# Kernel tuning notes

Hardware: AMD Instinct MI355X
Metric: run time of the kernel (lower is better)

Reference implementation:

```python
import jax, jax.numpy as jnp
import numpy as np

D_MODEL = 768
N_HEADS = 12
D_K = D_MODEL // N_HEADS

def setup_inputs() -> dict:
    key = jax.random.key(0)
    ks = jax.random.split(key, 9)
    B, S = 4, 2048
    s = 1.0 / np.sqrt(D_MODEL)
    return {
        "x": jax.random.normal(ks[0], (B, S, D_MODEL), dtype=jnp.float32),
        "Wq": jax.random.normal(ks[1], (D_MODEL, D_MODEL), dtype=jnp.float32) * s,
        "bq": jnp.zeros((D_MODEL,), dtype=jnp.float32),
        "Wk": jax.random.normal(ks[2], (D_MODEL, D_MODEL), dtype=jnp.float32) * s,
        "bk": jnp.zeros((D_MODEL,), dtype=jnp.float32),
        "Wv": jax.random.normal(ks[3], (D_MODEL, D_MODEL), dtype=jnp.float32) * s,
        "bv": jnp.zeros((D_MODEL,), dtype=jnp.float32),
        "Wo": jax.random.normal(ks[4], (D_MODEL, D_MODEL), dtype=jnp.float32) * s,
        "bo": jnp.zeros((D_MODEL,), dtype=jnp.float32),
    }

def reference(x, Wq, bq, Wk, bk, Wv, bv, Wo, bo):
    B, S, _ = x.shape
    # projections (nn.Linear: x @ W^T + b; here weights stored as (in, out) so x @ W + b)
    q = x @ Wq + bq
    k = x @ Wk + bk
    v = x @ Wv + bv
    # split heads -> (B, H, S, d_k)
    q = q.reshape(B, S, N_HEADS, D_K).transpose(0, 2, 1, 3)
    k = k.reshape(B, S, N_HEADS, D_K).transpose(0, 2, 1, 3)
    v = v.reshape(B, S, N_HEADS, D_K).transpose(0, 2, 1, 3)
    scores = jnp.einsum('bhqd,bhkd->bhqk', q, k) / jnp.sqrt(jnp.float32(D_K))
    causal = jnp.tril(jnp.ones((S, S), dtype=bool))  # True = keep
    scores = jnp.where(causal, scores, jnp.finfo(scores.dtype).min)
    weights = jax.nn.softmax(scores, axis=-1)  # dropout is identity in eval
    out = jnp.einsum('bhqk,bhkd->bhqd', weights, v)
    out = out.transpose(0, 2, 1, 3).reshape(B, S, D_MODEL)
    return out @ Wo + bo
```

## Files before the change

kernel.cpp:

```cpp
#include <hip/hip_runtime.h>
#include <hip/hip_bf16.h>

#define DM    768
#define HEADS 12
#define DK    64
#define SEQ   2048
#define BATCH 4
#define NE    ((size_t)BATCH * SEQ * DM)
#define KT    12
#define BRICK 8192

typedef short v8s __attribute__((ext_vector_type(8)));
typedef float v4f __attribute__((ext_vector_type(4)));

#define LDS_PTR(p) ((__attribute__((address_space(3))) unsigned int*)(p))
#define GLB_PTR(p) ((const __attribute__((address_space(1))) unsigned int*)(p))

__device__ __forceinline__ unsigned short f2bf(float f) {
    union { float f; unsigned u; } v; v.f = f;
    unsigned r = (v.u + 0x7FFFu + ((v.u >> 16) & 1u)) >> 16;
    return (unsigned short)r;
}
__device__ __forceinline__ unsigned pk2(float a, float b) {
    union { float f; unsigned u; } x, y; x.f = a; y.f = b;
    return (x.u >> 16) | (y.u & 0xFFFF0000u);
}
__device__ __forceinline__ unsigned pk2r(float a, float b) {
    return (unsigned)f2bf(a) | ((unsigned)f2bf(b) << 16);
}
__device__ __forceinline__ float fexp2(float x) {
#if __has_builtin(__builtin_amdgcn_exp2f)
    return __builtin_amdgcn_exp2f(x);
#else
    return __expf(x * 0.69314718056f);
#endif
}

#define QSCALE 0.18033688011112042f

__global__ __launch_bounds__(256)
void cvt_x_kernel(const float* __restrict__ x, unsigned short* __restrict__ xb) {
    const size_t p = ((size_t)blockIdx.x * 256 + threadIdx.x) * 8;
    const int m = (int)(p / DM);
    const int k = (int)(p % DM);
    const float4 a = *(const float4*)(x + p);
    const float4 b = *(const float4*)(x + p + 4);
    v8s o;
    o[0] = (short)f2bf(a.x); o[1] = (short)f2bf(a.y);
    o[2] = (short)f2bf(a.z); o[3] = (short)f2bf(a.w);
    o[4] = (short)f2bf(b.x); o[5] = (short)f2bf(b.y);
    o[6] = (short)f2bf(b.z); o[7] = (short)f2bf(b.w);
    const size_t dst = ((size_t)(m >> 7) * KT + (k >> 6)) * BRICK + (size_t)(m & 127) * 64 + (k & 63);
    *(v8s*)(xb + dst) = o;
}

__global__ __launch_bounds__(256)
void cvt_w_kernel(const float* __restrict__ W0, const float* __restrict__ W1,
                  const float* __restrict__ W2, const float* __restrict__ W3,
                  unsigned short* __restrict__ wt) {
    __shared__ unsigned short T[64][72];
    const int z = blockIdx.z;
    const float* W = (z == 0) ? W0 : (z == 1) ? W1 : (z == 2) ? W2 : W3;
    const float scale = (z == 0) ? QSCALE : 1.0f;
    const int k0 = blockIdx.x * 64, n0 = blockIdx.y * 64;
    const int t = threadIdx.x;
    {
        const int kr = t >> 2;
        const int ns = (t & 3) * 16;
        #pragma unroll
        for (int j = 0; j < 4; ++j) {
            const float4 v = *(const float4*)(W + (size_t)(k0 + kr) * DM + n0 + ns + j * 4);
            T[ns + j * 4 + 0][kr] = f2bf(v.x * scale);
            T[ns + j * 4 + 1][kr] = f2bf(v.y * scale);
            T[ns + j * 4 + 2][kr] = f2bf(v.z * scale);
            T[ns + j * 4 + 3][kr] = f2bf(v.w * scale);
        }
    }
    __syncthreads();
    {
        unsigned short* dst = wt + (size_t)z * DM * DM +
            ((size_t)(n0 >> 7) * KT + (k0 >> 6)) * BRICK + (size_t)(n0 & 64) * 64;
        const int n = t >> 2;
        const int ks = (t & 3) * 16;
        #pragma unroll
        for (int j = 0; j < 2; ++j)
            *(v8s*)(dst + (size_t)n * 64 + ks + j * 8) = *(const v8s*)&T[n][ks + j * 8];
    }
}

__global__ __launch_bounds__(256)
void gemm_qkv_kernel(const unsigned short* __restrict__ xb, const unsigned short* __restrict__ wtbuf,
                     const float* __restrict__ bq, const float* __restrict__ bk,
                     const float* __restrict__ bv,
                     unsigned short* __restrict__ qb, unsigned short* __restrict__ kb,
                     unsigned short* __restrict__ vtb) {
    __shared__ unsigned short smem[32768];
    const int idx = blockIdx.x;
    const int xcd = idx & 7, g = idx >> 3;
    const int mb = xcd + 8 * (g & 7);
    const int yb = g >> 3;
    const int z = yb / 6;
    const int N0 = (yb % 6) * 128;
    const float* bias = (z == 0) ? bq : (z == 1) ? bk : bv;
    const float bscale = (z == 0) ? QSCALE : 1.0f;

    const int t = threadIdx.x;
    const int w = t >> 6, lane = t & 63, quad = lane >> 4, l15 = lane & 15;
    const int wm = w >> 1, wn = w & 1;
    const int M0 = mb * 128;

    const unsigned short* gA = xb + (size_t)mb * (KT * BRICK);
    const unsigned short* gB = wtbuf + (size_t)yb * (KT * BRICK);

    const int r8 = lane >> 3;
    const int c8 = (lane & 7) ^ r8;
    const int goff = r8 * 64 + c8 * 8;
    const int rl = l15 & 7, rh = l15 >> 3;

    v4f acc[4][4];
    #pragma unroll
    for (int i = 0; i < 4; ++i)
        #pragma unroll
        for (int j = 0; j < 4; ++j) acc[i][j] = (v4f){0, 0, 0, 0};

    #pragma unroll
    for (int u = 0; u < 4; ++u) {
        const int win = w * 4 + u;
        __builtin_amdgcn_global_load_lds(GLB_PTR(gA + win * 512 + goff), LDS_PTR(smem + win * 512), 16, 0, 0);
        __builtin_amdgcn_global_load_lds(GLB_PTR(gB + win * 512 + goff), LDS_PTR(smem + 16384 + win * 512), 16, 0, 0);
    }
    __syncthreads();

    for (int kt = 0; kt < KT; ++kt) {
        const int cur = kt & 1;
        if (kt + 1 < KT) {
            const unsigned short* ta = gA + (kt + 1) * BRICK;
            const unsigned short* tb = gB + (kt + 1) * BRICK;
            const int nb = (1 - cur) * 8192;
            #pragma unroll
            for (int u = 0; u < 4; ++u) {
                const int win = w * 4 + u;
                __builtin_amdgcn_global_load_lds(GLB_PTR(ta + win * 512 + goff), LDS_PTR(smem + nb + win * 512), 16, 0, 0);
                __builtin_amdgcn_global_load_lds(GLB_PTR(tb + win * 512 + goff), LDS_PTR(smem + 16384 + nb + win * 512), 16, 0, 0);
            }
        }
        const unsigned short* As = smem + cur * 8192;
        const unsigned short* Bs = smem + 16384 + cur * 8192;
        #pragma unroll
        for (int kc = 0; kc < 2; ++kc) {
            const int cs = ((kc << 2) | quad) ^ rl;
            v8s a[4], b[4];
            #pragma unroll
            for (int i = 0; i < 4; ++i)
                a[i] = *(const v8s*)&As[(wm * 8 + i * 2 + rh) * 512 + rl * 64 + cs * 8];
            #pragma unroll
            for (int j = 0; j < 4; ++j)
                b[j] = *(const v8s*)&Bs[(wn * 8 + j * 2 + rh) * 512 + rl * 64 + cs * 8];
            #pragma unroll
            for (int i = 0; i < 4; ++i)
                #pragma unroll
                for (int j = 0; j < 4; ++j)
                    acc[i][j] = __builtin_amdgcn_mfma_f32_16x16x32_bf16(a[i], b[j], acc[i][j], 0, 0, 0);
        }
        __syncthreads();
    }

    const int b_ = M0 >> 11;
    const int sidx0 = M0 & 2047;
    const int h0 = N0 >> 6;

    if (z < 2) {
        unsigned short* outp = (z == 0) ? qb : kb;
        #pragma unroll
        for (int j = 0; j < 4; ++j) {
            const int n = N0 + wn * 64 + j * 16 + l15;
            const int h = n >> 6, d = n & 63;
            const float bv_ = bias[n] * bscale;
            #pragma unroll
            for (int i = 0; i < 4; ++i)
                #pragma unroll
                for (int r = 0; r < 4; ++r) {
                    const int sidx = sidx0 + wm * 64 + i * 16 + quad * 4 + r;
                    outp[(((size_t)(b_ * HEADS + h) * SEQ + sidx) << 6) + d] = f2bf(acc[i][j][r] + bv_);
                }
        }
    } else {
        unsigned short* Ts = smem;
        #pragma unroll
        for (int p = 0; p < 2; ++p) {
            __syncthreads();
            if (wm == p) {
                #pragma unroll
                for (int j = 0; j < 4; ++j) {
                    const int dloc = wn * 64 + j * 16 + l15;
                    const float bv_ = bias[N0 + dloc];
                    #pragma unroll
                    for (int i = 0; i < 4; ++i)
                        #pragma unroll
                        for (int r = 0; r < 4; ++r)
                            Ts[dloc * 72 + i * 16 + quad * 4 + r] = f2bf(acc[i][j][r] + bv_);
                }
            }
            __syncthreads();
            const int dloc = t >> 1, ms = (t & 1) * 32;
            const int h = h0 + (dloc >> 6), d = dloc & 63;
            unsigned short* dst = vtb + (((size_t)(b_ * HEADS + h) * DK + d) << 11) + sidx0 + p * 64 + ms;
            #pragma unroll
            for (int jj = 0; jj < 4; ++jj)
                *(v8s*)(dst + jj * 8) = *(const v8s*)&Ts[dloc * 72 + ms + jj * 8];
        }
    }
}

__global__ __launch_bounds__(256)
void gemm_out_kernel(const unsigned short* __restrict__ ob, const unsigned short* __restrict__ wto,
                     const float* __restrict__ bias, float* __restrict__ out) {
    __shared__ unsigned short smem[32768];
    const int idx = blockIdx.x;
    const int xcd = idx & 7, g = idx >> 3;
    const int mb = xcd + 8 * (g & 7);
    const int nb = g >> 3;
    const int t = threadIdx.x;
    const int w = t >> 6, lane = t & 63, quad = lane >> 4, l15 = lane & 15;
    const int wm = w >> 1, wn = w & 1;
    const int M0 = mb * 128;
    const int N0 = nb * 128;

    const unsigned short* gA = ob + (size_t)mb * (KT * BRICK);
    const unsigned short* gB = wto + (size_t)nb * (KT * BRICK);

    const int r8 = lane >> 3;
    const int c8 = (lane & 7) ^ r8;
    const int goff = r8 * 64 + c8 * 8;
    const int rl = l15 & 7, rh = l15 >> 3;

    v4f acc[4][4];
    #pragma unroll
    for (int i = 0; i < 4; ++i)
        #pragma unroll
        for (int j = 0; j < 4; ++j) acc[i][j] = (v4f){0, 0, 0, 0};

    #pragma unroll
    for (int u = 0; u < 4; ++u) {
        const int win = w * 4 + u;
        __builtin_amdgcn_global_load_lds(GLB_PTR(gA + win * 512 + goff), LDS_PTR(smem + win * 512), 16, 0, 0);
        __builtin_amdgcn_global_load_lds(GLB_PTR(gB + win * 512 + goff), LDS_PTR(smem + 16384 + win * 512), 16, 0, 0);
    }
    __syncthreads();

    for (int kt = 0; kt < KT; ++kt) {
        const int cur = kt & 1;
        if (kt + 1 < KT) {
            const unsigned short* ta = gA + (kt + 1) * BRICK;
            const unsigned short* tb = gB + (kt + 1) * BRICK;
            const int nxt = (1 - cur) * 8192;
            #pragma unroll
            for (int u = 0; u < 4; ++u) {
                const int win = w * 4 + u;
                __builtin_amdgcn_global_load_lds(GLB_PTR(ta + win * 512 + goff), LDS_PTR(smem + nxt + win * 512), 16, 0, 0);
                __builtin_amdgcn_global_load_lds(GLB_PTR(tb + win * 512 + goff), LDS_PTR(smem + 16384 + nxt + win * 512), 16, 0, 0);
            }
        }
        const unsigned short* As = smem + cur * 8192;
        const unsigned short* Bs = smem + 16384 + cur * 8192;
        #pragma unroll
        for (int kc = 0; kc < 2; ++kc) {
            const int cs = ((kc << 2) | quad) ^ rl;
            v8s a[4], b[4];
            #pragma unroll
            for (int i = 0; i < 4; ++i)
                a[i] = *(const v8s*)&As[(wm * 8 + i * 2 + rh) * 512 + rl * 64 + cs * 8];
            #pragma unroll
            for (int j = 0; j < 4; ++j)
                b[j] = *(const v8s*)&Bs[(wn * 8 + j * 2 + rh) * 512 + rl * 64 + cs * 8];
            #pragma unroll
            for (int i = 0; i < 4; ++i)
                #pragma unroll
                for (int j = 0; j < 4; ++j)
                    acc[i][j] = __builtin_amdgcn_mfma_f32_16x16x32_bf16(a[i], b[j], acc[i][j], 0, 0, 0);
        }
        __syncthreads();
    }

    #pragma unroll
    for (int j = 0; j < 4; ++j) {
        const int n = N0 + wn * 64 + j * 16 + l15;
        const float bv_ = bias[n];
        #pragma unroll
        for (int i = 0; i < 4; ++i)
            #pragma unroll
            for (int r = 0; r < 4; ++r) {
                const int m = M0 + wm * 64 + i * 16 + quad * 4 + r;
                out[(size_t)m * DM + n] = acc[i][j][r] + bv_;
            }
    }
}

__global__ __launch_bounds__(256, 5)
void attn_kernel(const unsigned short* __restrict__ Q, const unsigned short* __restrict__ K,
                 const unsigned short* __restrict__ VT, unsigned short* __restrict__ O) {
    __shared__ unsigned short smem[16384];
    unsigned short* Kb = smem;
    unsigned short* Vb = smem + 4096;
    unsigned short* Ps = smem + 8192;
    const int t = threadIdx.x;
    const int w = t >> 6, lane = t & 63, quad = lane >> 4, l15 = lane & 15;
    const int e7 = l15 & 7;

    const int idx = blockIdx.x;
    const int xcd = idx & 7;
    const int g   = idx >> 3;
    const int bh  = xcd + 8 * (g % 6);
    const int s   = 31 - g / 6;
    const int q0  = s * 64;
    const int nkt = s + 1;
    const size_t kvbase = (size_t)bh * SEQ * DK;

    v8s qf[2];
    #pragma unroll
    for (int c = 0; c < 2; ++c)
        qf[c] = *(const v8s*)(Q + kvbase + (size_t)(q0 + w * 16 + l15) * DK + c * 32 + quad * 8);

    v4f o[4];
    #pragma unroll
    for (int nf = 0; nf < 4; ++nf) o[nf] = (v4f){0, 0, 0, 0};
    v4f os = (v4f){0, 0, 0, 0};
    const v4f zero4 = (v4f){0, 0, 0, 0};

    const short one_bf = (short)0x3F80;
    const v8s ones = (v8s){one_bf, one_bf, one_bf, one_bf, one_bf, one_bf, one_bf, one_bf};

    const int srow = t >> 3;
    const int sc16 = t & 7;
    const int scolsw = (sc16 ^ (srow & 7)) * 8;
    const int gcol = sc16 * 8;
    const int so0 = srow * 64 + scolsw;
    const int so1 = (srow + 32) * 64 + scolsw;

    v8s kr0 = *(const v8s*)(K  + kvbase + (size_t)srow * DK + gcol);
    v8s kr1 = *(const v8s*)(K  + kvbase + (size_t)(srow + 32) * DK + gcol);
    v8s vr0 = *(const v8s*)(VT + kvbase + ((size_t)srow << 11) + gcol);
    v8s vr1 = *(const v8s*)(VT + kvbase + ((size_t)(srow + 32) << 11) + gcol);
    *(v8s*)&Kb[so0] = kr0;
    *(v8s*)&Kb[so1] = kr1;
    *(v8s*)&Vb[so0] = vr0;
    *(v8s*)&Vb[so1] = vr1;
    __syncthreads();

    const int q_ = q0 + w * 16 + l15;
    unsigned short* Pw = Ps + w * 1024;

    for (int kt = 0; kt < nkt; ++kt) {
        const int k0 = kt * 64;
        if (kt + 1 < nkt) {
            const int kn = k0 + 64;
            kr0 = *(const v8s*)(K  + kvbase + (size_t)(kn + srow) * DK + gcol);
            kr1 = *(const v8s*)(K  + kvbase + (size_t)(kn + srow + 32) * DK + gcol);
            vr0 = *(const v8s*)(VT + kvbase + ((size_t)srow << 11) + kn + gcol);
            vr1 = *(const v8s*)(VT + kvbase + ((size_t)(srow + 32) << 11) + kn + gcol);
        }

        v4f sc[4];
        #pragma unroll
        for (int s4 = 0; s4 < 4; ++s4) {
            const v8s kf = *(const v8s*)&Kb[(s4 * 16 + l15) * 64 + (quad ^ e7) * 8];
            sc[s4] = __builtin_amdgcn_mfma_f32_16x16x32_bf16(kf, qf[0], zero4, 0, 0, 0);
        }
        #pragma unroll
        for (int s4 = 0; s4 < 4; ++s4) {
            const v8s kf = *(const v8s*)&Kb[(s4 * 16 + l15) * 64 + ((4 | quad) ^ e7) * 8];
            sc[s4] = __builtin_amdgcn_mfma_f32_16x16x32_bf16(kf, qf[1], sc[s4], 0, 0, 0);
        }

        {
            const bool msk = (kt == s);
            #pragma unroll
            for (int s4 = 0; s4 < 4; ++s4) {
                float p[4];
                #pragma unroll
                for (int r = 0; r < 4; ++r) p[r] = fexp2(sc[s4][r]);
                if (msk) {
                    #pragma unroll
                    for (int r = 0; r < 4; ++r) {
                        const int key = k0 + s4 * 16 + quad * 4 + r;
                        if (key > q_) p[r] = 0.f;
                    }
                }
                uint2 pkv; pkv.x = pk2(p[0], p[1]); pkv.y = pk2(p[2], p[3]);
                const int col8 = (s4 * 4 + quad) ^ (e7 << 1);
                *(uint2*)&Pw[l15 * 64 + col8 * 4] = pkv;
            }
        }

        #pragma unroll
        for (int kc = 0; kc < 2; ++kc) {
            const int c16 = ((kc * 4 + quad) ^ e7) * 8;
            const v8s pf = *(const v8s*)&Pw[l15 * 64 + c16];
            os = __builtin_amdgcn_mfma_f32_16x16x32_bf16(ones, pf, os, 0, 0, 0);
            #pragma unroll
            for (int nf = 0; nf < 4; ++nf) {
                const v8s vf = *(const v8s*)&Vb[(nf * 16 + l15) * 64 + c16];
                o[nf] = __builtin_amdgcn_mfma_f32_16x16x32_bf16(vf, pf, o[nf], 0, 0, 0);
            }
        }

        if (kt + 1 < nkt) {
            __syncthreads();
            *(v8s*)&Kb[so0] = kr0;
            *(v8s*)&Kb[so1] = kr1;
            *(v8s*)&Vb[so0] = vr0;
            *(v8s*)&Vb[so1] = vr1;
            __syncthreads();
        }
    }

    const float inv = 1.f / os[0];

    const int b = bh / HEADS, h = bh % HEADS;
    const size_t br = ((size_t)(b * 16 + (q0 >> 7)) * KT + h) * BRICK;
    const int rowl = (q0 & 127) + w * 16 + l15;
    #pragma unroll
    for (int nf = 0; nf < 4; ++nf) {
        uint2 a2;
        a2.x = pk2r(o[nf][0] * inv, o[nf][1] * inv);
        a2.y = pk2r(o[nf][2] * inv, o[nf][3] * inv);
        *(uint2*)(O + br + (size_t)rowl * 64 + nf * 16 + quad * 4) = a2;
    }
}

extern "C" void kernel_launch(void* const* d_in, const int* in_sizes, int n_in,
                              void* d_out, int out_size, void* d_ws, size_t ws_size,
                              hipStream_t stream) {
    const float* x  = (const float*)d_in[0];
    const float* Wq = (const float*)d_in[1];
    const float* bq = (const float*)d_in[2];
    const float* Wk = (const float*)d_in[3];
    const float* bk = (const float*)d_in[4];
    const float* Wv = (const float*)d_in[5];
    const float* bv = (const float*)d_in[6];
    const float* Wo = (const float*)d_in[7];
    const float* bo = (const float*)d_in[8];
    float* out = (float*)d_out;

    unsigned short* xb  = (unsigned short*)d_ws;
    unsigned short* qb  = xb  + NE;
    unsigned short* kb  = qb  + NE;
    unsigned short* vtb = kb  + NE;
    unsigned short* wt  = vtb + NE;
    unsigned short* ob  = xb;

    cvt_x_kernel<<<dim3(NE / (8 * 256)), 256, 0, stream>>>(x, xb);
    cvt_w_kernel<<<dim3(12, 12, 4), 256, 0, stream>>>(Wq, Wk, Wv, Wo, wt);
    gemm_qkv_kernel<<<dim3(1152), 256, 0, stream>>>(xb, wt, bq, bk, bv, qb, kb, vtb);
    attn_kernel<<<dim3(1536), 256, 0, stream>>>(qb, kb, vtb, ob);
    gemm_out_kernel<<<dim3(384), 256, 0, stream>>>(ob, wt + (size_t)3 * DM * DM, bo, out);
}
```

Baseline: 200.4 us.

## Keep P in registers via 16x16x16 MFMA and double-buffer K/V tiles

```diff
diff --git a/kernel.cpp b/kernel.cpp
--- a/kernel.cpp
+++ b/kernel.cpp
@@ -10,6 +10,7 @@
 #define KT    12
 #define BRICK 8192
 
+typedef short v4s __attribute__((ext_vector_type(4)));
 typedef short v8s __attribute__((ext_vector_type(8)));
 typedef float v4f __attribute__((ext_vector_type(4)));
 
@@ -33,6 +34,17 @@
     return __builtin_amdgcn_exp2f(x);
 #else
     return __expf(x * 0.69314718056f);
+#endif
+}
+__device__ __forceinline__ v4f mfma16(v4s a, v4s b, v4f c) {
+#if __has_builtin(__builtin_amdgcn_mfma_f32_16x16x16_bf16)
+    return __builtin_amdgcn_mfma_f32_16x16x16_bf16(a, b, c, 0, 0, 0);
+#elif __has_builtin(__builtin_amdgcn_mfma_f32_16x16x16bf16_1k)
+    return __builtin_amdgcn_mfma_f32_16x16x16bf16_1k(a, b, c, 0, 0, 0);
+#else
+    v4f d;
+    asm("v_mfma_f32_16x16x16_bf16 %0, %1, %2, %3" : "=&v"(d) : "v"(a), "v"(b), "v"(c));
+    return d;
 #endif
 }
 
@@ -300,12 +312,10 @@
 void attn_kernel(const unsigned short* __restrict__ Q, const unsigned short* __restrict__ K,
                  const unsigned short* __restrict__ VT, unsigned short* __restrict__ O) {
     __shared__ unsigned short smem[16384];
-    unsigned short* Kb = smem;
-    unsigned short* Vb = smem + 4096;
-    unsigned short* Ps = smem + 8192;
     const int t = threadIdx.x;
     const int w = t >> 6, lane = t & 63, quad = lane >> 4, l15 = lane & 15;
     const int e7 = l15 & 7;
+    const int q1 = quad >> 1, q0x = quad & 1;
 
     const int idx = blockIdx.x;
     const int xcd = idx & 7;
@@ -328,7 +338,7 @@
     const v4f zero4 = (v4f){0, 0, 0, 0};
 
     const short one_bf = (short)0x3F80;
-    const v8s ones = (v8s){one_bf, one_bf, one_bf, one_bf, one_bf, one_bf, one_bf, one_bf};
+    const v4s ones4 = (v4s){one_bf, one_bf, one_bf, one_bf};
 
     const int srow = t >> 3;
     const int sc16 = t & 7;
@@ -341,15 +351,15 @@
     v8s kr1 = *(const v8s*)(K  + kvbase + (size_t)(srow + 32) * DK + gcol);
     v8s vr0 = *(const v8s*)(VT + kvbase + ((size_t)srow << 11) + gcol);
     v8s vr1 = *(const v8s*)(VT + kvbase + ((size_t)(srow + 32) << 11) + gcol);
-    *(v8s*)&Kb[so0] = kr0;
-    *(v8s*)&Kb[so1] = kr1;
-    *(v8s*)&Vb[so0] = vr0;
-    *(v8s*)&Vb[so1] = vr1;
+    *(v8s*)&smem[so0]        = kr0;
+    *(v8s*)&smem[so1]        = kr1;
+    *(v8s*)&smem[8192 + so0] = vr0;
+    *(v8s*)&smem[8192 + so1] = vr1;
     __syncthreads();
 
     const int q_ = q0 + w * 16 + l15;
-    unsigned short* Pw = Ps + w * 1024;
-
+
+    int cur = 0;
     for (int kt = 0; kt < nkt; ++kt) {
         const int k0 = kt * 64;
         if (kt + 1 < nkt) {
@@ -359,19 +369,22 @@
             vr0 = *(const v8s*)(VT + kvbase + ((size_t)srow << 11) + kn + gcol);
             vr1 = *(const v8s*)(VT + kvbase + ((size_t)(srow + 32) << 11) + kn + gcol);
         }
+        const unsigned short* Kc = smem + cur * 4096;
+        const unsigned short* Vc = smem + 8192 + cur * 4096;
 
         v4f sc[4];
         #pragma unroll
         for (int s4 = 0; s4 < 4; ++s4) {
-            const v8s kf = *(const v8s*)&Kb[(s4 * 16 + l15) * 64 + (quad ^ e7) * 8];
+            const v8s kf = *(const v8s*)&Kc[(s4 * 16 + l15) * 64 + ((quad ^ e7) << 3)];
             sc[s4] = __builtin_amdgcn_mfma_f32_16x16x32_bf16(kf, qf[0], zero4, 0, 0, 0);
         }
         #pragma unroll
         for (int s4 = 0; s4 < 4; ++s4) {
-            const v8s kf = *(const v8s*)&Kb[(s4 * 16 + l15) * 64 + ((4 | quad) ^ e7) * 8];
+            const v8s kf = *(const v8s*)&Kc[(s4 * 16 + l15) * 64 + (((4 | quad) ^ e7) << 3)];
             sc[s4] = __builtin_amdgcn_mfma_f32_16x16x32_bf16(kf, qf[1], sc[s4], 0, 0, 0);
         }
 
+        v4s pa[4];
         {
             const bool msk = (kt == s);
             #pragma unroll
@@ -386,46 +399,48 @@
                         if (key > q_) p[r] = 0.f;
                     }
                 }
-                uint2 pkv; pkv.x = pk2(p[0], p[1]); pkv.y = pk2(p[2], p[3]);
-                const int col8 = (s4 * 4 + quad) ^ (e7 << 1);
-                *(uint2*)&Pw[l15 * 64 + col8 * 4] = pkv;
-            }
-        }
-
-        #pragma unroll
-        for (int kc = 0; kc < 2; ++kc) {
-            const int c16 = ((kc * 4 + quad) ^ e7) * 8;
-            const v8s pf = *(const v8s*)&Pw[l15 * 64 + c16];
-            os = __builtin_amdgcn_mfma_f32_16x16x32_bf16(ones, pf, os, 0, 0, 0);
-            #pragma unroll
-            for (int nf = 0; nf < 4; ++nf) {
-                const v8s vf = *(const v8s*)&Vb[(nf * 16 + l15) * 64 + c16];
-                o[nf] = __builtin_amdgcn_mfma_f32_16x16x32_bf16(vf, pf, o[nf], 0, 0, 0);
-            }
-        }
+                union { unsigned u[2]; v4s s; } pu;
+                pu.u[0] = pk2(p[0], p[1]); pu.u[1] = pk2(p[2], p[3]);
+                pa[s4] = pu.s;
+            }
+        }
+
+        #pragma unroll
+        for (int nf = 0; nf < 4; ++nf) {
+            const int rowb = (nf * 16 + l15) * 64;
+            #pragma unroll
+            for (int s4 = 0; s4 < 4; ++s4) {
+                const v4s vb = *(const v4s*)&Vc[rowb + (((2 * s4 + q1) ^ e7) << 3) + (q0x << 2)];
+                o[nf] = mfma16(pa[s4], vb, o[nf]);
+            }
+        }
+        #pragma unroll
+        for (int s4 = 0; s4 < 4; ++s4)
+            os = mfma16(pa[s4], ones4, os);
 
         if (kt + 1 < nkt) {
-            __syncthreads();
-            *(v8s*)&Kb[so0] = kr0;
-            *(v8s*)&Kb[so1] = kr1;
-            *(v8s*)&Vb[so0] = vr0;
-            *(v8s*)&Vb[so1] = vr1;
-            __syncthreads();
-        }
-    }
-
-    const float inv = 1.f / os[0];
+            const int nb = (cur ^ 1) * 4096;
+            *(v8s*)&smem[nb + so0]        = kr0;
+            *(v8s*)&smem[nb + so1]        = kr1;
+            *(v8s*)&smem[8192 + nb + so0] = vr0;
+            *(v8s*)&smem[8192 + nb + so1] = vr1;
+        }
+        __syncthreads();
+        cur ^= 1;
+    }
+
+    float inv[4];
+    #pragma unroll
+    for (int r = 0; r < 4; ++r) inv[r] = 1.f / os[r];
 
     const int b = bh / HEADS, h = bh % HEADS;
     const size_t br = ((size_t)(b * 16 + (q0 >> 7)) * KT + h) * BRICK;
-    const int rowl = (q0 & 127) + w * 16 + l15;
-    #pragma unroll
-    for (int nf = 0; nf < 4; ++nf) {
-        uint2 a2;
-        a2.x = pk2r(o[nf][0] * inv, o[nf][1] * inv);
-        a2.y = pk2r(o[nf][2] * inv, o[nf][3] * inv);
-        *(uint2*)(O + br + (size_t)rowl * 64 + nf * 16 + quad * 4) = a2;
-    }
+    const int rowb = (q0 & 127) + w * 16 + quad * 4;
+    #pragma unroll
+    for (int nf = 0; nf < 4; ++nf)
+        #pragma unroll
+        for (int r = 0; r < 4; ++r)
+            O[br + (size_t)(rowb + r) * 64 + nf * 16 + l15] = f2bf(o[nf][r] * inv[r]);
 }
 
 extern "C" void kernel_launch(void* const* d_in, const int* in_sizes, int n_in,
```

Measured after the change: 206.6 us. +3.1%, slower.
